# Kernel optimization log

Hardware: AMD Instinct MI355X
Metric: run time of the kernel (lower is better)

Reference implementation:

```python
import jax, jax.numpy as jnp
import numpy as np

V, D, NL, S, B = 32000, 1024, 2, 2048, 1
EXPAND, N, K = 2, 16, 4
DI = EXPAND * D
EPS = 1e-5


def setup_inputs() -> dict:
    key = jax.random.key(0)
    ks = jax.random.split(key, 10)
    std = 0.02
    inp = {
        "input_ids": jax.random.randint(ks[0], (B, S), 0, V),
        "embedding": jax.random.normal(ks[1], (V, D), jnp.float32) * std,
        "in_proj_w": jax.random.normal(ks[2], (NL, 2 * DI, D), jnp.float32) * std,
        "conv_w": jax.random.normal(ks[3], (NL, DI, 1, K), jnp.float32) * std,
        "conv_b": jnp.zeros((NL, DI), jnp.float32),
        "x_proj_w": jax.random.normal(ks[4], (NL, 2 * N, DI), jnp.float32) * std,
        "dt_proj_w": jax.random.normal(ks[5], (NL, DI, DI), jnp.float32) * std,
        "dt_proj_b": jnp.zeros((NL, DI), jnp.float32),
        "A_log": jnp.broadcast_to(jnp.log(jnp.arange(1, N + 1, dtype=jnp.float32)), (NL, DI, N)).copy(),
        "D_param": jnp.ones((NL, DI), jnp.float32),
        "out_proj_w": jax.random.normal(ks[6], (NL, D, DI), jnp.float32) * std,
        "norm_w": jnp.ones((NL, D), jnp.float32),
        "norm_f_w": jnp.ones((D,), jnp.float32),
        "lm_head_w": jax.random.normal(ks[7], (V, D), jnp.float32) * std,
    }
    return inp


def rmsnorm(x, w):
    rms = jnp.sqrt(jnp.mean(x * x, axis=-1, keepdims=True) + EPS)
    return x / rms * w


def silu(x):
    return x * jax.nn.sigmoid(x)


def ssm_layer(x, in_w, cw, cb, xp_w, dt_w, dt_b, A_log, Dp):
    b, s, _ = x.shape
    xz = jnp.einsum("bsd,ed->bse", x, in_w)  # (B,S,2*DI)
    xi, z = jnp.split(xz, 2, axis=-1)
    # depthwise causal conv1d
    xc = jnp.swapaxes(xi, 1, 2)  # (B,DI,S)
    xc = jax.lax.conv_general_dilated(
        xc, cw, window_strides=(1,), padding=[(K - 1, 0)],
        dimension_numbers=("NCH", "OIH", "NCH"), feature_group_count=DI,
    ) + cb[None, :, None]
    xi = silu(jnp.swapaxes(xc, 1, 2))  # (B,S,DI)
    bc = jnp.einsum("bsd,ed->bse", xi, xp_w)  # (B,S,2N)
    Bc, Cc = jnp.split(bc, 2, axis=-1)
    dt = jax.nn.softplus(jnp.einsum("bsd,ed->bse", xi, dt_w) + dt_b)
    A = -jnp.exp(A_log)  # (DI,N)
    dA = jnp.exp(dt[..., None] * A)                      # (B,S,DI,N)
    dBu = dt[..., None] * Bc[:, :, None, :] * xi[..., None]  # (B,S,DI,N)

    def step(h, t):
        dA_t, dBu_t, C_t, u_t = t
        h = dA_t * h + dBu_t                     # (B,DI,N)
        y = jnp.sum(h * C_t[:, None, :], axis=-1) + Dp * u_t  # (B,DI)
        return h, y

    xs = (jnp.swapaxes(dA, 0, 1), jnp.swapaxes(dBu, 0, 1),
          jnp.swapaxes(Cc, 0, 1), jnp.swapaxes(xi, 0, 1))
    h0 = jnp.zeros((b, DI, N), x.dtype)
    _, ys = jax.lax.scan(step, h0, xs)
    y = jnp.swapaxes(ys, 0, 1)  # (B,S,DI)
    y = y * silu(z)
    return y


def reference(input_ids, embedding, in_proj_w, conv_w, conv_b, x_proj_w,
              dt_proj_w, dt_proj_b, A_log, D_param, out_proj_w, norm_w,
              norm_f_w, lm_head_w):
    x = embedding[input_ids]  # (B,S,D)
    for l in range(NL):
        h = rmsnorm(x, norm_w[l])
        y = ssm_layer(h, in_proj_w[l], conv_w[l], conv_b[l], x_proj_w[l],
                      dt_proj_w[l], dt_proj_b[l], A_log[l], D_param[l])
        x = x + jnp.einsum("bse,de->bsd", y, out_proj_w[l])
    x = rmsnorm(x, norm_f_w)
    logits = jnp.einsum("bsd,vd->bsv", x, lm_head_w)
    return logits
```

## Files before the change

### kernel.cpp

```cpp
#include <hip/hip_runtime.h>
#include <hip/hip_bf16.h>
#include <stdint.h>
#include <stddef.h>

#define Vv   32000
#define Dd   1024
#define NLay 2
#define Ss   2048
#define Nn   16
#define Kc   4
#define DIc  2048
#define EPSf 1e-5f
#define LCH  32
#define NCHc (Ss / LCH)
#define CATR 2176

typedef __attribute__((ext_vector_type(8))) short bf16x8;
typedef __attribute__((ext_vector_type(4))) float f32x4;

__device__ __forceinline__ short f2bf(float f) {
  union { float f; unsigned u; } a; a.f = f;
  return (short)((a.u + 0x7FFFu + ((a.u >> 16) & 1u)) >> 16);
}
__device__ __forceinline__ float bf2f(short s) {
  union { unsigned u; float f; } a; a.u = ((unsigned)(unsigned short)s) << 16;
  return a.f;
}
__device__ __forceinline__ int hswz(int r) { return (r & 3) ^ ((r >> 2) & 3); }

struct CvtSeg { const float* s; short* d; unsigned n4; };
struct CvtBatch { CvtSeg seg[7]; unsigned tot4; };
__global__ __launch_bounds__(256) void cvt_all_k(CvtBatch b) {
  for (unsigned idx = blockIdx.x * 256 + threadIdx.x; idx < b.tot4;
       idx += gridDim.x * 256) {
    unsigned r = idx;
    int sg = 0;
    while (sg < 6 && r >= b.seg[sg].n4) { r -= b.seg[sg].n4; ++sg; }
    float4 v = ((const float4*)b.seg[sg].s)[r];
    short4 o;
    o.x = f2bf(v.x); o.y = f2bf(v.y); o.z = f2bf(v.z); o.w = f2bf(v.w);
    ((short4*)b.seg[sg].d)[r] = o;
  }
}

__global__ __launch_bounds__(256) void embed_k(const int* __restrict__ ids,
                                               const float* __restrict__ emb,
                                               float* __restrict__ x) {
  int s = blockIdx.x;
  int id = ids[s];
  const float4* src = (const float4*)(emb + (size_t)id * Dd);
  float4* dst = (float4*)(x + (size_t)s * Dd);
  dst[threadIdx.x] = src[threadIdx.x];
}

__global__ __launch_bounds__(256) void rmsnorm_k(const float* __restrict__ x,
                                                 const float* __restrict__ w,
                                                 short* __restrict__ o) {
  int s = blockIdx.x, t = threadIdx.x;
  float4 v = ((const float4*)(x + (size_t)s * Dd))[t];
  float ss = v.x * v.x + v.y * v.y + v.z * v.z + v.w * v.w;
#pragma unroll
  for (int off = 32; off; off >>= 1) ss += __shfl_down(ss, off);
  __shared__ float red[4];
  if ((t & 63) == 0) red[t >> 6] = ss;
  __syncthreads();
  ss = red[0] + red[1] + red[2] + red[3];
  float rinv = rsqrtf(ss * (1.0f / Dd) + EPSf);
  float4 wv = ((const float4*)w)[t];
  short4 ov;
  ov.x = f2bf(v.x * rinv * wv.x);
  ov.y = f2bf(v.y * rinv * wv.y);
  ov.z = f2bf(v.z * rinv * wv.z);
  ov.w = f2bf(v.w * rinv * wv.w);
  ((short4*)(o + (size_t)s * Dd))[t] = ov;
}

template <int BM, int BN, int WM, int WN, bool RESID, bool CAT>
__global__ __launch_bounds__(WM * WN * 64, 2) void gemm_ring(
    const short* __restrict__ A, const short* __restrict__ B,
    float* C, const float* resb, float* C2, int M, int N, int K, int nMt) {
  constexpr int NT = WM * WN * 64;
  constexpr int FM = BM / (WM * 16);
  constexpr int FN = BN / (WN * 16);
  constexpr int PA = BM * 4 / NT;
  constexpr int PB = BN * 4 / NT;
  static_assert(PA + PB == 4, "vmcnt literals assume 4 loads per stage");
  __shared__ short lds[4][(BM + BN) * 32];
  const int t = threadIdx.x;
  const int lane = t & 63;
  const int w = t >> 6;
  const int wm = w / WN, wn = w % WN;
  const int lr = lane & 15, l4 = lane >> 4;
  const int nwg = gridDim.x;
  const int chunk = nwg >> 3;
  const int wg = (blockIdx.x & 7) * chunk + (blockIdx.x >> 3);
  const int mi = wg % nMt, ni = wg / nMt;
  const size_t rowBase = (size_t)mi * BM, colBase = (size_t)ni * BN;

  const short* aSrc[PA]; int aOff[PA];
  const short* bSrc[PB]; int bOff[PB];
#pragma unroll
  for (int p = 0; p < PA; ++p) {
    int q = p * NT + t;
    int row = q >> 2, s = q & 3;
    aSrc[p] = A + (rowBase + row) * K + ((s ^ hswz(row)) << 3);
    aOff[p] = q * 8;
  }
#pragma unroll
  for (int p = 0; p < PB; ++p) {
    int q = p * NT + t;
    int row = q >> 2, s = q & 3;
    bSrc[p] = B + (colBase + row) * K + ((s ^ hswz(row)) << 3);
    bOff[p] = BM * 32 + q * 8;
  }
  auto stage = [&](int buf, int k0) {
#pragma unroll
    for (int p = 0; p < PA; ++p)
      __builtin_amdgcn_global_load_lds(
          (__attribute__((address_space(1))) unsigned int*)(aSrc[p] + k0),
          (__attribute__((address_space(3))) unsigned int*)(&lds[buf][aOff[p]]), 16, 0, 0);
#pragma unroll
    for (int p = 0; p < PB; ++p)
      __builtin_amdgcn_global_load_lds(
          (__attribute__((address_space(1))) unsigned int*)(bSrc[p] + k0),
          (__attribute__((address_space(3))) unsigned int*)(&lds[buf][bOff[p]]), 16, 0, 0);
  };

  f32x4 acc[FM][FN];
#pragma unroll
  for (int i = 0; i < FM; i++)
#pragma unroll
    for (int j = 0; j < FN; j++) acc[i][j] = f32x4{0.f, 0.f, 0.f, 0.f};

  const int KT = K >> 5;
  stage(0, 0); stage(1, 32); stage(2, 64);
  for (int kt = 0; kt < KT; ++kt) {
    const int rem = KT - 1 - kt;
    __builtin_amdgcn_sched_barrier(0);
    if (rem >= 2)      asm volatile("s_waitcnt vmcnt(8)" ::: "memory");
    else if (rem == 1) asm volatile("s_waitcnt vmcnt(4)" ::: "memory");
    else               asm volatile("s_waitcnt vmcnt(0)" ::: "memory");
    __builtin_amdgcn_sched_barrier(0);
    __builtin_amdgcn_s_barrier();
    __builtin_amdgcn_sched_barrier(0);
    if (kt + 3 < KT) stage((kt + 3) & 3, (kt + 3) << 5);
    const short* la = &lds[kt & 3][0];
    const short* lb = &lds[kt & 3][BM * 32];
    bf16x8 av[FM], bv[FN];
#pragma unroll
    for (int i = 0; i < FM; i++) {
      int r = wm * (FM * 16) + i * 16 + lr;
      av[i] = *(const bf16x8*)&la[r * 32 + ((l4 ^ hswz(r)) << 3)];
    }
#pragma unroll
    for (int j = 0; j < FN; j++) {
      int r = wn * (FN * 16) + j * 16 + lr;
      bv[j] = *(const bf16x8*)&lb[r * 32 + ((l4 ^ hswz(r)) << 3)];
    }
    __builtin_amdgcn_s_setprio(1);
#pragma unroll
    for (int i = 0; i < FM; i++)
#pragma unroll
      for (int j = 0; j < FN; j++)
        acc[i][j] = __builtin_amdgcn_mfma_f32_16x16x32_bf16(av[i], bv[j], acc[i][j], 0, 0, 0);
    __builtin_amdgcn_s_setprio(0);
  }
#pragma unroll
  for (int i = 0; i < FM; i++) {
#pragma unroll
    for (int j = 0; j < FN; j++) {
      size_t r0 = rowBase + wm * (FM * 16) + i * 16 + l4 * 4;
      size_t c = colBase + wn * (FN * 16) + j * 16 + lr;
#pragma unroll
      for (int rr = 0; rr < 4; rr++) {
        size_t r = r0 + rr;
        float v = acc[i][j][rr];
        if (CAT) {
          if (c < DIc) {
            float xv = v + resb[c];
            C[r * DIc + c] = fmaxf(xv, 0.f) + log1pf(__expf(-fabsf(xv)));
          } else if (c < DIc + 2 * Nn) {
            C2[r * (2 * Nn) + (c - DIc)] = v;
          }
        } else {
          size_t idx = r * N + c;
          if (RESID) v += resb[idx];
          C[idx] = v;
        }
      }
    }
  }
}

__global__ __launch_bounds__(256) void conv_silu_k(const float* __restrict__ xz,
                                                   const float* __restrict__ cw,
                                                   const float* __restrict__ cb,
                                                   short* __restrict__ xiC) {
  int idx = blockIdx.x * 256 + threadIdx.x;
  int s = idx / (DIc / 4), c4 = idx - s * (DIc / 4);
  const float4* xz4 = (const float4*)xz;
  const size_t rstride = 2 * DIc / 4;
  float4 zero = {0.f, 0.f, 0.f, 0.f};
  float4 x0 = (s >= 3) ? xz4[(size_t)(s - 3) * rstride + c4] : zero;
  float4 x1 = (s >= 2) ? xz4[(size_t)(s - 2) * rstride + c4] : zero;
  float4 x2 = (s >= 1) ? xz4[(size_t)(s - 1) * rstride + c4] : zero;
  float4 x3 = xz4[(size_t)s * rstride + c4];
  float4 cbv = ((const float4*)cb)[c4];
  short4 ov;
  float xs[4][4] = {{x0.x, x1.x, x2.x, x3.x}, {x0.y, x1.y, x2.y, x3.y},
                    {x0.z, x1.z, x2.z, x3.z}, {x0.w, x1.w, x2.w, x3.w}};
  float cbs[4] = {cbv.x, cbv.y, cbv.z, cbv.w};
  short os[4];
#pragma unroll
  for (int j = 0; j < 4; j++) {
    float4 wv = ((const float4*)cw)[c4 * 4 + j];
    float acc = cbs[j] + wv.x * xs[j][0] + wv.y * xs[j][1] + wv.z * xs[j][2] + wv.w * xs[j][3];
    os[j] = f2bf(acc / (1.f + __expf(-acc)));
  }
  ov.x = os[0]; ov.y = os[1]; ov.z = os[2]; ov.w = os[3];
  ((short4*)xiC)[idx] = ov;
}

__global__ __launch_bounds__(256) void scan_pass1(const float* __restrict__ dt,
                                                  const short* __restrict__ u,
                                                  const float* __restrict__ bc,
                                                  const float* __restrict__ alog,
                                                  float* __restrict__ Ap,
                                                  float* __restrict__ Hl) {
  const int j = blockIdx.x;
  const int d = blockIdx.y * 256 + threadIdx.x;
  __shared__ float sB[LCH][Nn];
  for (int q = threadIdx.x; q < LCH * Nn; q += 256) {
    int tt = q >> 4, n = q & 15;
    sB[tt][n] = bc[(size_t)(j * LCH + tt) * 32 + n];
  }
  __syncthreads();
  float Ar[Nn], h[Nn], ap[Nn];
#pragma unroll
  for (int n = 0; n < Nn; n++) {
    Ar[n] = -__expf(alog[d * Nn + n]); h[n] = 0.f; ap[n] = 1.f;
  }
  const int t0 = j * LCH;
  for (int tt = 0; tt < LCH; tt++) {
    size_t gi = (size_t)(t0 + tt) * DIc + d;
    float dtv = dt[gi];
    float uv = bf2f(u[gi]);
    float dtu = dtv * uv;
#pragma unroll
    for (int n = 0; n < Nn; n++) {
      float a = __expf(dtv * Ar[n]);
      h[n] = a * h[n] + dtu * sB[tt][n];
      ap[n] *= a;
    }
  }
  size_t base = ((size_t)j * DIc + d) * Nn;
#pragma unroll
  for (int n = 0; n < Nn; n++) { Ap[base + n] = ap[n]; Hl[base + n] = h[n]; }
}

__global__ __launch_bounds__(256) void scan_combine(const float* __restrict__ Ap,
                                                    const float* __restrict__ Hl,
                                                    float* __restrict__ Hi) {
  int idx = blockIdx.x * 256 + threadIdx.x;
  float h = 0.f;
  for (int j = 0; j < NCHc; j++) {
    size_t o = (size_t)j * DIc * Nn + idx;
    Hi[o] = h;
    h = Ap[o] * h + Hl[o];
  }
}

__global__ __launch_bounds__(256) void scan_pass2(const float* __restrict__ dt,
                                                  const short* __restrict__ u,
                                                  const float* __restrict__ bc,
                                                  const float* __restrict__ alog,
                                                  const float* __restrict__ Hinit,
                                                  const float* __restrict__ Dp,
                                                  const float* __restrict__ xz,
                                                  short* __restrict__ y) {
  const int j = blockIdx.x;
  const int d = blockIdx.y * 256 + threadIdx.x;
  __shared__ float sB[LCH][Nn], sC[LCH][Nn];
  for (int q = threadIdx.x; q < LCH * Nn; q += 256) {
    int tt = q >> 4, n = q & 15;
    size_t r = (size_t)(j * LCH + tt) * 32;
    sB[tt][n] = bc[r + n];
    sC[tt][n] = bc[r + 16 + n];
  }
  __syncthreads();
  float Ar[Nn], h[Nn];
  size_t hb = ((size_t)j * DIc + d) * Nn;
#pragma unroll
  for (int n = 0; n < Nn; n++) {
    Ar[n] = -__expf(alog[d * Nn + n]); h[n] = Hinit[hb + n];
  }
  float dp = Dp[d];
  const int t0 = j * LCH;
  for (int tt = 0; tt < LCH; tt++) {
    size_t gi = (size_t)(t0 + tt) * DIc + d;
    float dtv = dt[gi];
    float uv = bf2f(u[gi]);
    float dtu = dtv * uv;
    float yv = dp * uv;
#pragma unroll
    for (int n = 0; n < Nn; n++) {
      float a = __expf(dtv * Ar[n]);
      h[n] = a * h[n] + dtu * sB[tt][n];
      yv += h[n] * sC[tt][n];
    }
    float zv = xz[(size_t)(t0 + tt) * (2 * DIc) + DIc + d];
    float sz = zv / (1.f + __expf(-zv));
    y[gi] = f2bf(yv * sz);
  }
}

extern "C" void kernel_launch(void* const* d_in, const int* in_sizes, int n_in,
                              void* d_out, int out_size, void* d_ws, size_t ws_size,
                              hipStream_t stream) {
  (void)in_sizes; (void)n_in; (void)out_size; (void)ws_size;
  const int* ids = (const int*)d_in[0];
  const float* emb = (const float*)d_in[1];
  const float* in_proj_w = (const float*)d_in[2];
  const float* conv_w = (const float*)d_in[3];
  const float* conv_b = (const float*)d_in[4];
  const float* x_proj_w = (const float*)d_in[5];
  const float* dt_proj_w = (const float*)d_in[6];
  const float* dt_proj_b = (const float*)d_in[7];
  const float* A_log = (const float*)d_in[8];
  const float* D_param = (const float*)d_in[9];
  const float* out_proj_w = (const float*)d_in[10];
  const float* norm_w = (const float*)d_in[11];
  const float* norm_f_w = (const float*)d_in[12];
  const float* lm_head_w = (const float*)d_in[13];
  float* logits = (float*)d_out;

  char* ws = (char*)d_ws;
  size_t woff = 0;
  auto walloc = [&](size_t bytes) { void* p = ws + woff; woff += (bytes + 255) & ~(size_t)255; return p; };
  float* x     = (float*)walloc((size_t)Ss * Dd * 4);
  short* xfbf  = (short*)walloc((size_t)Ss * Dd * 2);
  short* w_lm  = (short*)walloc((size_t)Vv * Dd * 2);

  char* sc = (char*)d_out;
  size_t soff = 0;
  auto salloc = [&](size_t bytes) { void* p = sc + soff; soff += (bytes + 255) & ~(size_t)255; return p; };
  float* xz   = (float*)salloc((size_t)Ss * 2 * DIc * 4);
  float* dtb  = (float*)salloc((size_t)Ss * DIc * 4);
  float* bc   = (float*)salloc((size_t)Ss * 32 * 4);
  float* Ap   = (float*)salloc((size_t)NCHc * DIc * Nn * 4);
  float* Hl   = (float*)salloc((size_t)NCHc * DIc * Nn * 4);
  float* Hi   = (float*)salloc((size_t)NCHc * DIc * Nn * 4);
  short* hbf  = (short*)salloc((size_t)Ss * Dd * 2);
  short* xiC  = (short*)salloc((size_t)Ss * DIc * 2);
  short* ybf  = (short*)salloc((size_t)Ss * DIc * 2);
  short* w_in = (short*)salloc((size_t)NLay * 2 * DIc * Dd * 2);
  short* w_cat= (short*)salloc((size_t)NLay * CATR * DIc * 2);
  short* w_out= (short*)salloc((size_t)NLay * Dd * DIc * 2);

  CvtBatch cb2{};
  unsigned tot = 0;
  auto addseg = [&](int i, const float* s, short* d, size_t n) {
    cb2.seg[i].s = s; cb2.seg[i].d = d; cb2.seg[i].n4 = (unsigned)(n / 4);
    tot += (unsigned)(n / 4);
  };
  addseg(0, in_proj_w, w_in, (size_t)NLay * 2 * DIc * Dd);
  addseg(1, out_proj_w, w_out, (size_t)NLay * Dd * DIc);
  addseg(2, lm_head_w, w_lm, (size_t)Vv * Dd);
  addseg(3, dt_proj_w, w_cat, (size_t)DIc * DIc);
  addseg(4, x_proj_w, w_cat + (size_t)DIc * DIc, (size_t)2 * Nn * DIc);
  addseg(5, dt_proj_w + (size_t)DIc * DIc, w_cat + (size_t)CATR * DIc, (size_t)DIc * DIc);
  addseg(6, x_proj_w + (size_t)2 * Nn * DIc,
         w_cat + (size_t)CATR * DIc + (size_t)DIc * DIc, (size_t)2 * Nn * DIc);
  cb2.tot4 = tot;
  cvt_all_k<<<dim3(4096), dim3(256), 0, stream>>>(cb2);

  embed_k<<<dim3(Ss), dim3(256), 0, stream>>>(ids, emb, x);

  for (int l = 0; l < NLay; l++) {
    rmsnorm_k<<<dim3(Ss), dim3(256), 0, stream>>>(x, norm_w + (size_t)l * Dd, hbf);
    gemm_ring<128, 128, 2, 2, false, false><<<dim3(512), dim3(256), 0, stream>>>(
        hbf, w_in + (size_t)l * 2 * DIc * Dd, xz, nullptr, nullptr, Ss, 2 * DIc, Dd, 16);
    conv_silu_k<<<dim3(Ss * DIc / 4 / 256), dim3(256), 0, stream>>>(
        xz, conv_w + (size_t)l * DIc * Kc, conv_b + (size_t)l * DIc, xiC);
    gemm_ring<128, 128, 2, 2, false, true><<<dim3(272), dim3(256), 0, stream>>>(
        xiC, w_cat + (size_t)l * CATR * DIc, dtb, dt_proj_b + (size_t)l * DIc, bc,
        Ss, CATR, DIc, 16);
    scan_pass1<<<dim3(NCHc, DIc / 256), dim3(256), 0, stream>>>(
        dtb, xiC, bc, A_log + (size_t)l * DIc * Nn, Ap, Hl);
    scan_combine<<<dim3(DIc * Nn / 256), dim3(256), 0, stream>>>(Ap, Hl, Hi);
    scan_pass2<<<dim3(NCHc, DIc / 256), dim3(256), 0, stream>>>(
        dtb, xiC, bc, A_log + (size_t)l * DIc * Nn, Hi,
        D_param + (size_t)l * DIc, xz, ybf);
    gemm_ring<128, 128, 2, 2, true, false><<<dim3(128), dim3(256), 0, stream>>>(
        ybf, w_out + (size_t)l * Dd * DIc, x, x, nullptr, Ss, Dd, DIc, 16);
  }

  rmsnorm_k<<<dim3(Ss), dim3(256), 0, stream>>>(x, norm_f_w, xfbf);
  gemm_ring<256, 256, 2, 4, false, false><<<dim3(1000), dim3(512), 0, stream>>>(
      xfbf, w_lm, logits, nullptr, nullptr, Ss, Vv, Dd, 8);
}
```

Before: 659.7 us.

## Interleave A/B global-to-LDS loads with split MFMA phases in 512-thread GEMM

For GEMM configurations with 512 threads, each K-step is split into two halves. The prefetch of the A tile is issued between the first half's LDS reads and its MFMAs, and the prefetch of the B tile between the second half's reads and its MFMAs, with extra workgroup barriers around each phase. This sandwich schedule aims to spread global-load issue across the MFMA work and keep the matrix units busy. In exchange it adds several barriers per iteration and lgkmcnt(0) waits. The vmcnt accounting may also shift because A and B loads are now issued at different times.

Result: no change. 664.5 us (+0.7%).

```diff
diff --git a/kernel.cpp b/kernel.cpp
--- a/kernel.cpp
+++ b/kernel.cpp
@@ -84,6 +84,7 @@
   constexpr int FN = BN / (WN * 16);
   constexpr int PA = BM * 4 / NT;
   constexpr int PB = BN * 4 / NT;
+  constexpr bool SAND = (NT == 512);
   static_assert(PA + PB == 4, "vmcnt literals assume 4 loads per stage");
   __shared__ short lds[4][(BM + BN) * 32];
   const int t = threadIdx.x;
@@ -113,12 +114,14 @@
     bSrc[p] = B + (colBase + row) * K + ((s ^ hswz(row)) << 3);
     bOff[p] = BM * 32 + q * 8;
   }
-  auto stage = [&](int buf, int k0) {
+  auto stageA = [&](int buf, int k0) {
 #pragma unroll
     for (int p = 0; p < PA; ++p)
       __builtin_amdgcn_global_load_lds(
           (__attribute__((address_space(1))) unsigned int*)(aSrc[p] + k0),
           (__attribute__((address_space(3))) unsigned int*)(&lds[buf][aOff[p]]), 16, 0, 0);
+  };
+  auto stageB = [&](int buf, int k0) {
 #pragma unroll
     for (int p = 0; p < PB; ++p)
       __builtin_amdgcn_global_load_lds(
@@ -133,7 +136,9 @@
     for (int j = 0; j < FN; j++) acc[i][j] = f32x4{0.f, 0.f, 0.f, 0.f};
 
   const int KT = K >> 5;
-  stage(0, 0); stage(1, 32); stage(2, 64);
+  stageA(0, 0); stageB(0, 0);
+  stageA(1, 32); stageB(1, 32);
+  stageA(2, 64); stageB(2, 64);
   for (int kt = 0; kt < KT; ++kt) {
     const int rem = KT - 1 - kt;
     __builtin_amdgcn_sched_barrier(0);
@@ -143,27 +148,75 @@
     __builtin_amdgcn_sched_barrier(0);
     __builtin_amdgcn_s_barrier();
     __builtin_amdgcn_sched_barrier(0);
-    if (kt + 3 < KT) stage((kt + 3) & 3, (kt + 3) << 5);
     const short* la = &lds[kt & 3][0];
     const short* lb = &lds[kt & 3][BM * 32];
-    bf16x8 av[FM], bv[FN];
-#pragma unroll
-    for (int i = 0; i < FM; i++) {
-      int r = wm * (FM * 16) + i * 16 + lr;
-      av[i] = *(const bf16x8*)&la[r * 32 + ((l4 ^ hswz(r)) << 3)];
+
+    if constexpr (SAND) {
+      constexpr int FH = FM / 2;
+      bf16x8 av0[FH], bv[FN];
+#pragma unroll
+      for (int j = 0; j < FN; j++) {
+        int r = wn * (FN * 16) + j * 16 + lr;
+        bv[j] = *(const bf16x8*)&lb[r * 32 + ((l4 ^ hswz(r)) << 3)];
+      }
+#pragma unroll
+      for (int i = 0; i < FH; i++) {
+        int r = wm * (FM * 16) + i * 16 + lr;
+        av0[i] = *(const bf16x8*)&la[r * 32 + ((l4 ^ hswz(r)) << 3)];
+      }
+      if (kt + 3 < KT) stageA((kt + 3) & 3, (kt + 3) << 5);
+      __builtin_amdgcn_s_barrier();
+      asm volatile("s_waitcnt lgkmcnt(0)" ::: "memory");
+      __builtin_amdgcn_sched_barrier(0);
+      __builtin_amdgcn_s_setprio(1);
+#pragma unroll
+      for (int i = 0; i < FH; i++)
+#pragma unroll
+        for (int j = 0; j < FN; j++)
+          acc[i][j] = __builtin_amdgcn_mfma_f32_16x16x32_bf16(av0[i], bv[j], acc[i][j], 0, 0, 0);
+      __builtin_amdgcn_s_setprio(0);
+      __builtin_amdgcn_sched_barrier(0);
+      __builtin_amdgcn_s_barrier();
+      bf16x8 av1[FH];
+#pragma unroll
+      for (int i = 0; i < FH; i++) {
+        int r = wm * (FM * 16) + (FH + i) * 16 + lr;
+        av1[i] = *(const bf16x8*)&la[r * 32 + ((l4 ^ hswz(r)) << 3)];
+      }
+      if (kt + 3 < KT) stageB((kt + 3) & 3, (kt + 3) << 5);
+      __builtin_amdgcn_s_barrier();
+      asm volatile("s_waitcnt lgkmcnt(0)" ::: "memory");
+      __builtin_amdgcn_sched_barrier(0);
+      __builtin_amdgcn_s_setprio(1);
+#pragma unroll
+      for (int i = 0; i < FH; i++)
+#pragma unroll
+        for (int j = 0; j < FN; j++)
+          acc[FH + i][j] = __builtin_amdgcn_mfma_f32_16x16x32_bf16(av1[i], bv[j], acc[FH + i][j], 0, 0, 0);
+      __builtin_amdgcn_s_setprio(0);
+      __builtin_amdgcn_sched_barrier(0);
+      __builtin_amdgcn_s_barrier();
+    } else {
+      if (kt + 3 < KT) { stageA((kt + 3) & 3, (kt + 3) << 5); stageB((kt + 3) & 3, (kt + 3) << 5); }
+      bf16x8 av[FM], bv[FN];
+#pragma unroll
+      for (int i = 0; i < FM; i++) {
+        int r = wm * (FM * 16) + i * 16 + lr;
+        av[i] = *(const bf16x8*)&la[r * 32 + ((l4 ^ hswz(r)) << 3)];
+      }
+#pragma unroll
+      for (int j = 0; j < FN; j++) {
+        int r = wn * (FN * 16) + j * 16 + lr;
+        bv[j] = *(const bf16x8*)&lb[r * 32 + ((l4 ^ hswz(r)) << 3)];
+      }
+      __builtin_amdgcn_s_setprio(1);
+#pragma unroll
+      for (int i = 0; i < FM; i++)
+#pragma unroll
+        for (int j = 0; j < FN; j++)
+          acc[i][j] = __builtin_amdgcn_mfma_f32_16x16x32_bf16(av[i], bv[j], acc[i][j], 0, 0, 0);
+      __builtin_amdgcn_s_setprio(0);
     }
-#pragma unroll
-    for (int j = 0; j < FN; j++) {
-      int r = wn * (FN * 16) + j * 16 + lr;
-      bv[j] = *(const bf16x8*)&lb[r * 32 + ((l4 ^ hswz(r)) << 3)];
-    }
-    __builtin_amdgcn_s_setprio(1);
-#pragma unroll
-    for (int i = 0; i < FM; i++)
-#pragma unroll
-      for (int j = 0; j < FN; j++)
-        acc[i][j] = __builtin_amdgcn_mfma_f32_16x16x32_bf16(av[i], bv[j], acc[i][j], 0, 0, 0);
-    __builtin_amdgcn_s_setprio(0);
   }
 #pragma unroll
   for (int i = 0; i < FM; i++) {
```

## Replace LM-head GEMM with 8-phase pipelined global_load_lds kernel

Applied to the files above, without the earlier changes.

Adds a dedicated 256x256-tile bf16 GEMM for the LM head. It stages tiles directly from global to LDS with global_load_lds into two buffers and an XOR swizzle. Loads are interleaved with MFMA phases using explicit waitcnt, barriers and setprio, and workgroups are remapped across XCDs. The aim is to hide global-load latency and raise MFMA utilisation on the largest GEMM, at the cost of fragile hand scheduling.

New measurement: 657.5 us. About the same (-0.3%).

```diff
diff --git a/kernel.cpp b/kernel.cpp
--- a/kernel.cpp
+++ b/kernel.cpp
@@ -192,6 +192,129 @@
   }
 }
 
+__global__ __launch_bounds__(512, 1) void gemm8p(const short* __restrict__ A,
+                                                 const short* __restrict__ B,
+                                                 float* __restrict__ C,
+                                                 int M, int N, int K, int nMt) {
+  __shared__ short lds[2][512 * 64];
+  const int t = threadIdx.x;
+  const int lane = t & 63;
+  const int w = t >> 6;
+  const int wm = w >> 2, wn = w & 3;
+  const int lr = lane & 15, l4 = lane >> 4;
+  const int nwg = gridDim.x, chunk = nwg >> 3;
+  const int wg = (blockIdx.x & 7) * chunk + (blockIdx.x >> 3);
+  const int mi = wg % nMt, ni = wg / nMt;
+  const size_t rowBase = (size_t)mi * 256, colBase = (size_t)ni * 256;
+
+  const short* gsrc[4][2];
+  int loff[4][2];
+#pragma unroll
+  for (int sub = 0; sub < 4; ++sub)
+#pragma unroll
+    for (int u = 0; u < 2; ++u) {
+      int q = u * 512 + t;
+      int rbase = (sub >= 2) ? 128 : 0;
+      int row = rbase + (q >> 3);
+      int s = q & 7;
+      bool isA = (sub == 0 || sub == 3);
+      const short* bp = isA ? (A + (rowBase + row) * (size_t)K)
+                            : (B + (colBase + row) * (size_t)K);
+      gsrc[sub][u] = bp + ((s ^ (row & 7)) << 3);
+      loff[sub][u] = (isA ? 0 : 256 * 64) + rbase * 64 + q * 8;
+    }
+
+#define STG8(subc, dbufc, kb)                                                      \
+  {                                                                                \
+    __builtin_amdgcn_global_load_lds(                                              \
+        (__attribute__((address_space(1))) unsigned int*)(gsrc[subc][0] + (kb)),   \
+        (__attribute__((address_space(3))) unsigned int*)(&lds[dbufc][loff[subc][0]]), 16, 0, 0); \
+    __builtin_amdgcn_global_load_lds(                                              \
+        (__attribute__((address_space(1))) unsigned int*)(gsrc[subc][1] + (kb)),   \
+        (__attribute__((address_space(3))) unsigned int*)(&lds[dbufc][loff[subc][1]]), 16, 0, 0); \
+  }
+
+  f32x4 acc[8][4];
+#pragma unroll
+  for (int i = 0; i < 8; i++)
+#pragma unroll
+    for (int j = 0; j < 4; j++) acc[i][j] = f32x4{0.f, 0.f, 0.f, 0.f};
+
+  const int nMac = K >> 7;
+  STG8(0, 0, 0) STG8(1, 0, 0) STG8(2, 0, 0) STG8(3, 0, 0)
+  STG8(1, 1, 64) STG8(2, 1, 64)
+  asm volatile("s_waitcnt vmcnt(4)" ::: "memory");
+  __builtin_amdgcn_s_barrier();
+
+  bf16x8 bB[4];
+  for (int m = 0; m < nMac; ++m) {
+    const bool last = (m == nMac - 1);
+    const int kbOdd = (2 * m + 1) << 6;
+    const int kbE2 = (2 * m + 2) << 6;
+    const int kbO2 = (2 * m + 3) << 6;
+#pragma unroll
+    for (int p = 0; p < 8; ++p) {
+      const int tp = p >> 2;
+      const int pq = p & 3;
+      const int mh = pq & 1, kh = pq >> 1;
+      const short* lbase = &lds[tp][0];
+      bf16x8 a[4];
+      if (pq == 0 || pq == 2) {
+#pragma unroll
+        for (int j = 0; j < 4; ++j) {
+          int r = wn * 64 + j * 16 + lr;
+          int sidx = kh * 4 + l4;
+          bB[j] = *(const bf16x8*)&lbase[256 * 64 + r * 64 + ((sidx ^ (r & 7)) << 3)];
+        }
+      }
+#pragma unroll
+      for (int i = 0; i < 4; ++i) {
+        int r = wm * 128 + mh * 64 + i * 16 + lr;
+        int sidx = kh * 4 + l4;
+        a[i] = *(const bf16x8*)&lbase[r * 64 + ((sidx ^ (r & 7)) << 3)];
+      }
+      if (p == 0) { STG8(0, 1, kbOdd) STG8(3, 1, kbOdd) }
+      else if (p == 3) { if (!last) { STG8(1, 0, kbE2) STG8(2, 0, kbE2) } }
+      else if (p == 4) { if (!last) { STG8(0, 0, kbE2) STG8(3, 0, kbE2) } }
+      else if (p == 7) { if (!last) { STG8(1, 1, kbO2) STG8(2, 1, kbO2) } }
+      if (p == 3) {
+        __builtin_amdgcn_sched_barrier(0);
+        if (last) asm volatile("s_waitcnt vmcnt(0)" ::: "memory");
+        else      asm volatile("s_waitcnt vmcnt(4)" ::: "memory");
+        __builtin_amdgcn_sched_barrier(0);
+      } else if (p == 7 && !last) {
+        __builtin_amdgcn_sched_barrier(0);
+        asm volatile("s_waitcnt vmcnt(4)" ::: "memory");
+        __builtin_amdgcn_sched_barrier(0);
+      }
+      __builtin_amdgcn_s_barrier();
+      asm volatile("s_waitcnt lgkmcnt(0)" ::: "memory");
+      __builtin_amdgcn_sched_barrier(0);
+      __builtin_amdgcn_s_setprio(1);
+#pragma unroll
+      for (int i = 0; i < 4; ++i)
+#pragma unroll
+        for (int j = 0; j < 4; ++j)
+          acc[mh * 4 + i][j] =
+              __builtin_amdgcn_mfma_f32_16x16x32_bf16(a[i], bB[j], acc[mh * 4 + i][j], 0, 0, 0);
+      __builtin_amdgcn_s_setprio(0);
+      __builtin_amdgcn_sched_barrier(0);
+      __builtin_amdgcn_s_barrier();
+    }
+  }
+#pragma unroll
+  for (int i = 0; i < 8; i++) {
+#pragma unroll
+    for (int j = 0; j < 4; j++) {
+      size_t r0 = rowBase + wm * 128 + i * 16 + l4 * 4;
+      size_t c = colBase + wn * 64 + j * 16 + lr;
+#pragma unroll
+      for (int rr = 0; rr < 4; rr++)
+        C[(r0 + rr) * N + c] = acc[i][j][rr];
+    }
+  }
+}
+
 __global__ __launch_bounds__(256) void conv_silu_k(const float* __restrict__ xz,
                                                    const float* __restrict__ cw,
                                                    const float* __restrict__ cb,
@@ -396,6 +519,5 @@
   }
 
   rmsnorm_k<<<dim3(Ss), dim3(256), 0, stream>>>(x, norm_f_w, xfbf);
-  gemm_ring<256, 256, 2, 4, false, false><<<dim3(1000), dim3(512), 0, stream>>>(
-      xfbf, w_lm, logits, nullptr, nullptr, Ss, Vv, Dd, 8);
-}
+  gemm8p<<<dim3(1000), dim3(512), 0, stream>>>(xfbf, w_lm, logits, Ss, Vv, Dd, 8);
+}
```

## Fuse lm_head fp32-to-bf16 conversion into a dedicated LM-head GEMM

Applied to the files above, without the earlier changes.

Removes the separate conversion of the 32000x1024 lm_head weight to bf16 and drops its workspace buffer. A new GEMM kernel reads the fp32 B operand straight from global memory into registers, converts it, and writes it into swizzled LDS, while A still streams in through direct global-to-LDS loads. The aim is to save a full write and re-read of the converted weight. In exchange, the GEMM reads twice as many bytes for B and adds conversion ALU work inside the main loop, managed with hand-placed waitcnts.

Result: slower. 1.306 ms (+97.9%).

```diff
diff --git a/kernel.cpp b/kernel.cpp
--- a/kernel.cpp
+++ b/kernel.cpp
@@ -35,7 +35,7 @@
        idx += gridDim.x * 256) {
     unsigned r = idx;
     int sg = 0;
-    while (sg < 6 && r >= b.seg[sg].n4) { r -= b.seg[sg].n4; ++sg; }
+    while (sg < 5 && r >= b.seg[sg].n4) { r -= b.seg[sg].n4; ++sg; }
     float4 v = ((const float4*)b.seg[sg].s)[r];
     short4 o;
     o.x = f2bf(v.x); o.y = f2bf(v.y); o.z = f2bf(v.z); o.w = f2bf(v.w);
@@ -192,6 +192,141 @@
   }
 }
 
+__global__ __launch_bounds__(512, 1) void gemm_lm(const short* __restrict__ A,
+                                                  const float* __restrict__ Bf,
+                                                  float* __restrict__ C,
+                                                  int M, int N, int K, int nMt) {
+  __shared__ short lds[2][512 * 64];
+  const int t = threadIdx.x;
+  const int lane = t & 63;
+  const int w = t >> 6;
+  const int wm = w >> 2, wn = w & 3;
+  const int lr = lane & 15, l4 = lane >> 4;
+  const int nwg = gridDim.x, chunk = nwg >> 3;
+  const int wg = (blockIdx.x & 7) * chunk + (blockIdx.x >> 3);
+  const int mi = wg % nMt, ni = wg / nMt;
+  const size_t rowBase = (size_t)mi * 256, colBase = (size_t)ni * 256;
+
+  const short* aSrc[4]; int aOff[4];
+#pragma unroll
+  for (int p = 0; p < 4; ++p) {
+    int q = p * 512 + t;
+    int row = q >> 3, s = q & 7;
+    aSrc[p] = A + (rowBase + row) * (size_t)K + ((s ^ (row & 7)) << 3);
+    aOff[p] = q * 8;
+  }
+  auto stageA = [&](int buf, int k0) {
+#pragma unroll
+    for (int p = 0; p < 4; ++p)
+      __builtin_amdgcn_global_load_lds(
+          (__attribute__((address_space(1))) unsigned int*)(aSrc[p] + k0),
+          (__attribute__((address_space(3))) unsigned int*)(&lds[buf][aOff[p]]), 16, 0, 0);
+  };
+  const int brow = t >> 1, bhf = t & 1;
+  const float* bSrc = Bf + (colBase + brow) * (size_t)K + bhf * 32;
+  float4 s0[8], s1[8];
+  auto loadB = [&](float4 (&dst)[8], int k0) {
+    const float4* p4 = (const float4*)(bSrc + k0);
+#pragma unroll
+    for (int i = 0; i < 8; ++i) dst[i] = p4[i];
+  };
+  auto writeB = [&](float4 (&src)[8], int buf) {
+    short* base = &lds[buf][256 * 64 + brow * 64];
+#pragma unroll
+    for (int i2 = 0; i2 < 4; ++i2) {
+      float4 lo = src[i2 * 2], hi = src[i2 * 2 + 1];
+      bf16x8 v;
+      v[0] = f2bf(lo.x); v[1] = f2bf(lo.y); v[2] = f2bf(lo.z); v[3] = f2bf(lo.w);
+      v[4] = f2bf(hi.x); v[5] = f2bf(hi.y); v[6] = f2bf(hi.z); v[7] = f2bf(hi.w);
+      int slot = (4 * bhf + i2) ^ (brow & 7);
+      *(bf16x8*)(base + slot * 8) = v;
+    }
+  };
+
+  f32x4 acc[8][4];
+#pragma unroll
+  for (int i = 0; i < 8; i++)
+#pragma unroll
+    for (int j = 0; j < 4; j++) acc[i][j] = f32x4{0.f, 0.f, 0.f, 0.f};
+
+  const int KT = K >> 6;
+  loadB(s0, 0);
+  loadB(s1, 64);
+  stageA(0, 0);
+  __builtin_amdgcn_sched_barrier(0);
+  asm volatile("s_waitcnt vmcnt(12)" ::: "memory");
+  __builtin_amdgcn_sched_barrier(0);
+  writeB(s0, 0);
+  __builtin_amdgcn_sched_barrier(0);
+  asm volatile("s_waitcnt vmcnt(8) lgkmcnt(0)" ::: "memory");
+  __builtin_amdgcn_sched_barrier(0);
+  __builtin_amdgcn_s_barrier();
+
+  auto iter = [&](int kt, float4 (&bW)[8], float4 (&bL)[8]) {
+    const int cur = kt & 1, nxt = cur ^ 1;
+    const int rem = KT - 1 - kt;
+    if (rem >= 1) stageA(nxt, (kt + 1) << 6);
+    if (rem >= 2) loadB(bL, (kt + 2) << 6);
+    const short* la = &lds[cur][0];
+    const short* lb = &lds[cur][256 * 64];
+    bf16x8 av[8][2], bv[4][2];
+#pragma unroll
+    for (int i = 0; i < 8; ++i)
+#pragma unroll
+      for (int kq = 0; kq < 2; ++kq) {
+        int r = wm * 128 + i * 16 + lr;
+        int sidx = kq * 4 + l4;
+        av[i][kq] = *(const bf16x8*)&la[r * 64 + ((sidx ^ (r & 7)) << 3)];
+      }
+#pragma unroll
+    for (int j = 0; j < 4; ++j)
+#pragma unroll
+      for (int kq = 0; kq < 2; ++kq) {
+        int r = wn * 64 + j * 16 + lr;
+        int sidx = kq * 4 + l4;
+        bv[j][kq] = *(const bf16x8*)&lb[r * 64 + ((sidx ^ (r & 7)) << 3)];
+      }
+    if (rem >= 1) {
+      __builtin_amdgcn_sched_barrier(0);
+      if (rem >= 2) asm volatile("s_waitcnt vmcnt(12)" ::: "memory");
+      else          asm volatile("s_waitcnt vmcnt(4)" ::: "memory");
+      __builtin_amdgcn_sched_barrier(0);
+      writeB(bW, nxt);
+    }
+    __builtin_amdgcn_s_setprio(1);
+#pragma unroll
+    for (int kq = 0; kq < 2; ++kq)
+#pragma unroll
+      for (int i = 0; i < 8; ++i)
+#pragma unroll
+        for (int j = 0; j < 4; ++j)
+          acc[i][j] = __builtin_amdgcn_mfma_f32_16x16x32_bf16(av[i][kq], bv[j][kq], acc[i][j], 0, 0, 0);
+    __builtin_amdgcn_s_setprio(0);
+    if (rem >= 1) {
+      __builtin_amdgcn_sched_barrier(0);
+      if (rem >= 2) asm volatile("s_waitcnt vmcnt(8) lgkmcnt(0)" ::: "memory");
+      else          asm volatile("s_waitcnt vmcnt(0) lgkmcnt(0)" ::: "memory");
+      __builtin_amdgcn_sched_barrier(0);
+      __builtin_amdgcn_s_barrier();
+    }
+  };
+  for (int kt = 0; kt < KT; kt += 2) {
+    iter(kt, s1, s0);
+    iter(kt + 1, s0, s1);
+  }
+#pragma unroll
+  for (int i = 0; i < 8; i++) {
+#pragma unroll
+    for (int j = 0; j < 4; j++) {
+      size_t r0 = rowBase + wm * 128 + i * 16 + l4 * 4;
+      size_t c = colBase + wn * 64 + j * 16 + lr;
+#pragma unroll
+      for (int rr = 0; rr < 4; rr++)
+        C[(r0 + rr) * N + c] = acc[i][j][rr];
+    }
+  }
+}
+
 __global__ __launch_bounds__(256) void conv_silu_k(const float* __restrict__ xz,
                                                    const float* __restrict__ cw,
                                                    const float* __restrict__ cb,
@@ -339,7 +474,6 @@
   auto walloc = [&](size_t bytes) { void* p = ws + woff; woff += (bytes + 255) & ~(size_t)255; return p; };
   float* x     = (float*)walloc((size_t)Ss * Dd * 4);
   short* xfbf  = (short*)walloc((size_t)Ss * Dd * 2);
-  short* w_lm  = (short*)walloc((size_t)Vv * Dd * 2);
 
   char* sc = (char*)d_out;
   size_t soff = 0;
@@ -365,14 +499,13 @@
   };
   addseg(0, in_proj_w, w_in, (size_t)NLay * 2 * DIc * Dd);
   addseg(1, out_proj_w, w_out, (size_t)NLay * Dd * DIc);
-  addseg(2, lm_head_w, w_lm, (size_t)Vv * Dd);
-  addseg(3, dt_proj_w, w_cat, (size_t)DIc * DIc);
-  addseg(4, x_proj_w, w_cat + (size_t)DIc * DIc, (size_t)2 * Nn * DIc);
-  addseg(5, dt_proj_w + (size_t)DIc * DIc, w_cat + (size_t)CATR * DIc, (size_t)DIc * DIc);
-  addseg(6, x_proj_w + (size_t)2 * Nn * DIc,
+  addseg(2, dt_proj_w, w_cat, (size_t)DIc * DIc);
+  addseg(3, x_proj_w, w_cat + (size_t)DIc * DIc, (size_t)2 * Nn * DIc);
+  addseg(4, dt_proj_w + (size_t)DIc * DIc, w_cat + (size_t)CATR * DIc, (size_t)DIc * DIc);
+  addseg(5, x_proj_w + (size_t)2 * Nn * DIc,
          w_cat + (size_t)CATR * DIc + (size_t)DIc * DIc, (size_t)2 * Nn * DIc);
   cb2.tot4 = tot;
-  cvt_all_k<<<dim3(4096), dim3(256), 0, stream>>>(cb2);
+  cvt_all_k<<<dim3(2048), dim3(256), 0, stream>>>(cb2);
 
   embed_k<<<dim3(Ss), dim3(256), 0, stream>>>(ids, emb, x);
 
@@ -396,6 +529,5 @@
   }
 
   rmsnorm_k<<<dim3(Ss), dim3(256), 0, stream>>>(x, norm_f_w, xfbf);
-  gemm_ring<256, 256, 2, 4, false, false><<<dim3(1000), dim3(512), 0, stream>>>(
-      xfbf, w_lm, logits, nullptr, nullptr, Ss, Vv, Dd, 8);
-}
+  gemm_lm<<<dim3(1000), dim3(512), 0, stream>>>(xfbf, lm_head_w, logits, Ss, Vv, Dd, 8);
+}
```
